# Kernel optimization log

Hardware: AMD Instinct MI355X
Metric: run time of the kernel (lower is better)

Reference implementation:

```python
import jax, jax.numpy as jnp
from jax import lax
import numpy as np

B = 8192   # samples
L = 32     # predicted chars per sample (num_chars[i])
M = 32     # target labels per sample (num_labels[i])
C = 96     # character classes


def _edit_trace(pred, tgt):
    """Levenshtein DP + backtrace for one sample.
    pred: [L] int, tgt: [M] int.
    Returns (ti, tj, valid) of length L+M: 1-based (i,j) positions of the
    diagonal (match/substitute) moves on the optimal edit path, as emitted by
    distance_and_trace; valid masks non-diagonal / out-of-path steps."""
    Ls, Ms = pred.shape[0], tgt.shape[0]
    cost = (pred[:, None] != tgt[None, :]).astype(jnp.int32)  # [L,M]
    row0 = jnp.arange(Ms + 1, dtype=jnp.int32)

    def row_step(prev, crow):
        first = prev[0] + 1
        def col_step(left, z):
            up, diag, c = z
            v = jnp.minimum(jnp.minimum(up + 1, left + 1), diag + c)
            return v, v
        _, rest = lax.scan(col_step, first, (prev[1:], prev[:-1], crow))
        new = jnp.concatenate([first[None], rest])
        return new, new

    _, rows = lax.scan(row_step, row0, cost)
    D = jnp.concatenate([row0[None, :], rows], axis=0)  # [L+1, M+1]

    def bt_step(carry, _):
        i, j = carry
        c = cost[jnp.maximum(i - 1, 0), jnp.maximum(j - 1, 0)]
        dij = D[i, j]
        diag = (i > 0) & (j > 0) & (D[i - 1, j - 1] + c == dij)
        up = (~diag) & (i > 0) & (D[i - 1, j] + 1 == dij)
        left = (~diag) & (~up) & (j > 0)
        ni = i - (diag | up).astype(jnp.int32)
        nj = j - (diag | left).astype(jnp.int32)
        return (ni, nj), (i, j, diag)

    (_, _), (ti, tj, valid) = lax.scan(
        bt_step, (jnp.int32(Ls), jnp.int32(Ms)), None, length=Ls + Ms)
    return ti, tj, valid


def _forward(x, y, num_chars, num_labels):
    b = num_chars.shape[0]
    c = x.shape[1]
    l = x.shape[0] // b
    m = y.shape[0] // b
    logits = x.reshape(b, l, c)          # [B,L,C]
    labels = y.reshape(b, m)             # [B,M]
    pred = jnp.argmax(logits, axis=-1)   # torch.max(x,1) indices
    ti, tj, valid = jax.vmap(_edit_trace)(pred, labels)  # [B, L+M] each
    logp = jax.nn.log_softmax(logits, axis=-1)
    xi = jnp.where(valid, ti - 1, 0)     # trace[:,0]-1 (+ per-sample offset via reshape)
    yi = jnp.where(valid, tj - 1, 0)     # trace[:,1]-1
    lab = jnp.take_along_axis(labels, yi, axis=1)                 # [B,L+M]
    lp = jnp.take_along_axis(logp, xi[..., None], axis=1)         # [B,L+M,C]
    ce = -jnp.take_along_axis(lp, lab[..., None], axis=2)[..., 0]  # [B,L+M]
    cnt = valid.sum(axis=1)
    per_sample = jnp.where(valid, ce, 0.0).sum(axis=1) / jnp.maximum(cnt, 1)
    nonempty = cnt > 0                   # attenuation: skip empty traces
    total = jnp.where(nonempty, per_sample, 0.0).sum()
    return total / nonempty.sum()


def setup_inputs() -> dict:
    key = jax.random.key(0)
    k1, k2 = jax.random.split(key)
    x = jax.random.normal(k1, (B * L, C), dtype=jnp.float32)
    y = jax.random.randint(k2, (B * M,), 0, C, dtype=jnp.int32)
    num_chars = jnp.full((B,), L, dtype=jnp.int32)
    num_labels = jnp.full((B,), M, dtype=jnp.int32)
    return {"x": x, "y": y, "num_chars": num_chars, "num_labels": num_labels}


def reference(x, y, num_chars, num_labels):
    return _forward(x, y, num_chars, num_labels)
```

## Files before the change

### kernel.cpp

```cpp
#include <hip/hip_runtime.h>
#include <stdint.h>

#define BNUM  8192
#define LROWS 32
#define MLAB  32
#define CCLS  96
#define WPB   2
#define SPW   2
#define SPB   (WPB*SPW)
#define NBLK  (BNUM/SPB)

__global__ __launch_bounds__(128, 4) void editloss_main(
    const float* __restrict__ x, const int* __restrict__ y,
    float2* __restrict__ out_ws)
{
    __shared__ float  ceTab[SPB][LROWS * MLAB];
    __shared__ float2 lpS[SPB][LROWS];

    const int w    = threadIdx.x >> 6;
    const int lane = threadIdx.x & 63;
    const int g    = lane >> 5;
    const int u    = lane & 31;
    const int s    = w * SPW + g;
    const int sb   = blockIdx.x * SPB + s;

    const float* xs    = x + (size_t)sb * (LROWS * CCLS);
    const int    lab_u = y[sb * MLAB + u];

    const float4* rowv = (const float4*)(xs + (size_t)u * CCLS);
    float4 buf[24];
#pragma unroll
    for (int k = 0; k < 24; ++k) buf[k] = rowv[k];

    float gbuf[LROWS];
    {
        const float* gcol = xs + lab_u;
#pragma unroll
        for (int r = 0; r < LROWS; ++r) gbuf[r] = gcol[r * CCLS];
    }

    float mA = -1e30f, mB = -1e30f;
    int   iA = 0,      iB = 0;
    float sA = 0.f,    sB = 0.f;
#pragma unroll
    for (int k = 0; k < 12; ++k) {
        const float4 v = buf[k];
        const int base = k * 4;
        if (v.x > mA) { mA = v.x; iA = base + 0; }
        if (v.y > mA) { mA = v.y; iA = base + 1; }
        if (v.z > mA) { mA = v.z; iA = base + 2; }
        if (v.w > mA) { mA = v.w; iA = base + 3; }
        sA += __expf(v.x) + __expf(v.y) + __expf(v.z) + __expf(v.w);
    }
#pragma unroll
    for (int k = 0; k < 12; ++k) {
        const float4 v = buf[12 + k];
        const int base = 48 + k * 4;
        if (v.x > mB) { mB = v.x; iB = base + 0; }
        if (v.y > mB) { mB = v.y; iB = base + 1; }
        if (v.z > mB) { mB = v.z; iB = base + 2; }
        if (v.w > mB) { mB = v.w; iB = base + 3; }
        sB += __expf(v.x) + __expf(v.y) + __expf(v.z) + __expf(v.w);
    }
    const int   idx = (mB > mA) ? iB : iA;
    const float lse = __logf(sA + sB);
    lpS[s][u] = make_float2(lse, (float)idx);

#pragma unroll
    for (int r = 0; r < LROWS; r += 4)
        asm volatile("" : "+v"(gbuf[r]), "+v"(gbuf[r+1]),
                          "+v"(gbuf[r+2]), "+v"(gbuf[r+3]));

    asm volatile("s_waitcnt lgkmcnt(0)" ::: "memory");

#pragma unroll
    for (int r = 0; r < LROWS; ++r) {
        const float2 lp = lpS[s][r];
        const float  ce = lp.x - gbuf[r];
        ceTab[s][r * MLAB + u] = ((int)lp.y == lab_u) ? ce : -ce;
    }
    asm volatile("s_waitcnt lgkmcnt(0)" ::: "memory");

    const int j = u + 1;
    int   prevW = 0;   float prevCE = 0.f;
    int   diagW = 0;   float diagCE = 0.f;
#pragma unroll 4
    for (int d = 1; d <= LROWS + MLAB; ++d) {
        const int   lWs  = __shfl_up(prevW, 1);
        const float lCEs = __shfl_up(prevCE, 1);
        const int i = d - j;
        const int   lW  = (u == 0) ? max(i, 0)     : lWs;
        const float lCE = (u == 0) ? 0.f           : lCEs;
        const int   dW  = (u == 0) ? max(i - 1, 0) : diagW;
        const float dCE = (u == 0) ? 0.f           : diagCE;
        int curW; float curCE;
        if (i <= 0) {
            curW = j; curCE = 0.f;
        } else if (i > LROWS) {
            curW = prevW; curCE = prevCE;
        } else {
            const int uD = prevW & 255, uC = prevW >> 8;
            const int lD = lW & 255,    lC = lW >> 8;
            const int dD = dW & 255,    dC = dW >> 8;
            const float ct  = ceTab[s][(i - 1) * MLAB + u];
            const int   c   = (ct < 0.f) ? 1 : 0;
            const int nD = min(min(uD, lD) + 1, dD + c);
            const bool dg = (dD + c == nD);
            const bool up = !dg && (uD + 1 == nD);
            int nC; float nCE;
            if (dg)      { nC = dC + 1; nCE = dCE + fabsf(ct); }
            else if (up) { nC = uC;     nCE = prevCE;          }
            else         { nC = lC;     nCE = lCE;             }
            curW = nD | (nC << 8);
            curCE = nCE;
        }
        diagW = lWs; diagCE = lCEs;
        prevW = curW; prevCE = curCE;
    }

    if (u == 31) {
        const int cnt = prevW >> 8;
        out_ws[sb] = make_float2((cnt > 0) ? prevCE / (float)cnt : 0.f,
                                 (cnt > 0) ? 1.f : 0.f);
    }
}

__global__ __launch_bounds__(256) void editloss_finalize(
    const float2* __restrict__ ws, float* __restrict__ out)
{
    float s = 0.f, c = 0.f;
    for (int k = threadIdx.x; k < BNUM; k += 256) {
        const float2 v = ws[k];
        s += v.x; c += v.y;
    }
#pragma unroll
    for (int d = 32; d >= 1; d >>= 1) {
        s += __shfl_xor(s, d);
        c += __shfl_xor(c, d);
    }
    __shared__ float ss[4], cc[4];
    const int w = threadIdx.x >> 6, lane = threadIdx.x & 63;
    if (lane == 0) { ss[w] = s; cc[w] = c; }
    __syncthreads();
    if (threadIdx.x == 0) {
        const float S  = ss[0] + ss[1] + ss[2] + ss[3];
        const float C2 = cc[0] + cc[1] + cc[2] + cc[3];
        out[0] = (C2 > 0.f) ? (S / C2) : 0.f;
    }
}

extern "C" void kernel_launch(void* const* d_in, const int* in_sizes, int n_in,
                              void* d_out, int out_size, void* d_ws, size_t ws_size,
                              hipStream_t stream) {
    const float* x = (const float*)d_in[0];
    const int*   y = (const int*)d_in[1];
    float* out = (float*)d_out;

    float2* per_sample = (float2*)d_ws;

    editloss_main<<<NBLK, 128, 0, stream>>>(x, y, per_sample);
    editloss_finalize<<<1, 256, 0, stream>>>(per_sample, out);
}
```

Measured before the change: 171.9 us.

## Split row argmax/logsumexp into a separate wave-parallel kernel

```diff
diff --git a/kernel.cpp b/kernel.cpp
--- a/kernel.cpp
+++ b/kernel.cpp
@@ -5,14 +5,45 @@
 #define LROWS 32
 #define MLAB  32
 #define CCLS  96
+#define SPW   2
 #define WPB   2
-#define SPW   2
 #define SPB   (WPB*SPW)
-#define NBLK  (BNUM/SPB)
+#define NBLKB (BNUM/SPB)
 
-__global__ __launch_bounds__(128, 4) void editloss_main(
+__global__ __launch_bounds__(256) void editloss_rows(
+    const float* __restrict__ x, float2* __restrict__ lpG)
+{
+    const int w    = threadIdx.x >> 6;
+    const int lane = threadIdx.x & 63;
+    const int g    = lane >> 5;
+    const int u    = lane & 31;
+    const int rowbase = blockIdx.x * LROWS + w * 8;
+
+#pragma unroll
+    for (int t = 0; t < 4; ++t) {
+        const int r = rowbase + t * 2 + g;
+        const float* p = x + (size_t)r * CCLS + u * 3;
+        const float v0 = p[0], v1 = p[1], v2 = p[2];
+
+        float m = fmaxf(fmaxf(v0, v1), v2);
+#pragma unroll
+        for (int sft = 16; sft >= 1; sft >>= 1) m = fmaxf(m, __shfl_xor(m, sft));
+        int cand = (v0 == m) ? (u * 3)
+                 : (v1 == m) ? (u * 3 + 1)
+                 : (v2 == m) ? (u * 3 + 2) : 4096;
+#pragma unroll
+        for (int sft = 16; sft >= 1; sft >>= 1) cand = min(cand, __shfl_xor(cand, sft));
+        float se = __expf(v0) + __expf(v1) + __expf(v2);
+#pragma unroll
+        for (int sft = 16; sft >= 1; sft >>= 1) se += __shfl_xor(se, sft);
+
+        if (u == 0) lpG[r] = make_float2(__logf(se), (float)cand);
+    }
+}
+
+__global__ __launch_bounds__(128) void editloss_dp(
     const float* __restrict__ x, const int* __restrict__ y,
-    float2* __restrict__ out_ws)
+    const float2* __restrict__ lpG, float2* __restrict__ out_ws)
 {
     __shared__ float  ceTab[SPB][LROWS * MLAB];
     __shared__ float2 lpS[SPB][LROWS];
@@ -27,10 +58,7 @@
     const float* xs    = x + (size_t)sb * (LROWS * CCLS);
     const int    lab_u = y[sb * MLAB + u];
 
-    const float4* rowv = (const float4*)(xs + (size_t)u * CCLS);
-    float4 buf[24];
-#pragma unroll
-    for (int k = 0; k < 24; ++k) buf[k] = rowv[k];
+    lpS[s][u] = lpG[sb * LROWS + u];
 
     float gbuf[LROWS];
     {
@@ -38,38 +66,6 @@
 #pragma unroll
         for (int r = 0; r < LROWS; ++r) gbuf[r] = gcol[r * CCLS];
     }
-
-    float mA = -1e30f, mB = -1e30f;
-    int   iA = 0,      iB = 0;
-    float sA = 0.f,    sB = 0.f;
-#pragma unroll
-    for (int k = 0; k < 12; ++k) {
-        const float4 v = buf[k];
-        const int base = k * 4;
-        if (v.x > mA) { mA = v.x; iA = base + 0; }
-        if (v.y > mA) { mA = v.y; iA = base + 1; }
-        if (v.z > mA) { mA = v.z; iA = base + 2; }
-        if (v.w > mA) { mA = v.w; iA = base + 3; }
-        sA += __expf(v.x) + __expf(v.y) + __expf(v.z) + __expf(v.w);
-    }
-#pragma unroll
-    for (int k = 0; k < 12; ++k) {
-        const float4 v = buf[12 + k];
-        const int base = 48 + k * 4;
-        if (v.x > mB) { mB = v.x; iB = base + 0; }
-        if (v.y > mB) { mB = v.y; iB = base + 1; }
-        if (v.z > mB) { mB = v.z; iB = base + 2; }
-        if (v.w > mB) { mB = v.w; iB = base + 3; }
-        sB += __expf(v.x) + __expf(v.y) + __expf(v.z) + __expf(v.w);
-    }
-    const int   idx = (mB > mA) ? iB : iA;
-    const float lse = __logf(sA + sB);
-    lpS[s][u] = make_float2(lse, (float)idx);
-
-#pragma unroll
-    for (int r = 0; r < LROWS; r += 4)
-        asm volatile("" : "+v"(gbuf[r]), "+v"(gbuf[r+1]),
-                          "+v"(gbuf[r+2]), "+v"(gbuf[r+3]));
 
     asm volatile("s_waitcnt lgkmcnt(0)" ::: "memory");
 
@@ -156,8 +152,10 @@
     const int*   y = (const int*)d_in[1];
     float* out = (float*)d_out;
 
-    float2* per_sample = (float2*)d_ws;
+    float2* lpG        = (float2*)d_ws;
+    float2* per_sample = lpG + (size_t)BNUM * LROWS;
 
-    editloss_main<<<NBLK, 128, 0, stream>>>(x, y, per_sample);
+    editloss_rows<<<BNUM, 256, 0, stream>>>(x, lpG);
+    editloss_dp<<<NBLKB, 128, 0, stream>>>(x, y, lpG, per_sample);
     editloss_finalize<<<1, 256, 0, stream>>>(per_sample, out);
 }
```

Result: slower. 184.4 us (+7.3%).

## Stage logits through padded LDS tile with coalesced wave-wide loads

Applied to the files above, without the earlier changes.

```diff
diff --git a/kernel.cpp b/kernel.cpp
--- a/kernel.cpp
+++ b/kernel.cpp
@@ -5,81 +5,91 @@
 #define LROWS 32
 #define MLAB  32
 #define CCLS  96
-#define WPB   2
-#define SPW   2
-#define SPB   (WPB*SPW)
+#define CH    16
+#define PAD2  49
+#define WAVES 2
+#define SPWV  2
+#define SPB   (WAVES*SPWV)
 #define NBLK  (BNUM/SPB)
 
-__global__ __launch_bounds__(128, 4) void editloss_main(
+__global__ __launch_bounds__(128) void editloss_main(
     const float* __restrict__ x, const int* __restrict__ y,
     float2* __restrict__ out_ws)
 {
-    __shared__ float  ceTab[SPB][LROWS * MLAB];
-    __shared__ float2 lpS[SPB][LROWS];
+    __shared__ float2 xTile[WAVES][CH * PAD2];
+    __shared__ float  ceTab[WAVES][SPWV][LROWS*MLAB];
+    __shared__ float2 lpS  [WAVES][SPWV][LROWS];
 
-    const int w    = threadIdx.x >> 6;
+    const int wv   = threadIdx.x >> 6;
     const int lane = threadIdx.x & 63;
     const int g    = lane >> 5;
     const int u    = lane & 31;
-    const int s    = w * SPW + g;
-    const int sb   = blockIdx.x * SPB + s;
+    const int sb0  = (blockIdx.x * WAVES + wv) * SPWV;
 
-    const float* xs    = x + (size_t)sb * (LROWS * CCLS);
-    const int    lab_u = y[sb * MLAB + u];
+    for (int si = 0; si < SPWV; ++si) {
+        const float* xs = x + (size_t)(sb0 + si) * (LROWS * CCLS);
+        const int lab_u = y[(sb0 + si) * MLAB + u];
 
-    const float4* rowv = (const float4*)(xs + (size_t)u * CCLS);
-    float4 buf[24];
+        const float4* gsrc = (const float4*)xs;
+        float4 st[12];
 #pragma unroll
-    for (int k = 0; k < 24; ++k) buf[k] = rowv[k];
-
-    float gbuf[LROWS];
-    {
-        const float* gcol = xs + lab_u;
-#pragma unroll
-        for (int r = 0; r < LROWS; ++r) gbuf[r] = gcol[r * CCLS];
-    }
-
-    float mA = -1e30f, mB = -1e30f;
-    int   iA = 0,      iB = 0;
-    float sA = 0.f,    sB = 0.f;
-#pragma unroll
-    for (int k = 0; k < 12; ++k) {
-        const float4 v = buf[k];
-        const int base = k * 4;
-        if (v.x > mA) { mA = v.x; iA = base + 0; }
-        if (v.y > mA) { mA = v.y; iA = base + 1; }
-        if (v.z > mA) { mA = v.z; iA = base + 2; }
-        if (v.w > mA) { mA = v.w; iA = base + 3; }
-        sA += __expf(v.x) + __expf(v.y) + __expf(v.z) + __expf(v.w);
-    }
-#pragma unroll
-    for (int k = 0; k < 12; ++k) {
-        const float4 v = buf[12 + k];
-        const int base = 48 + k * 4;
-        if (v.x > mB) { mB = v.x; iB = base + 0; }
-        if (v.y > mB) { mB = v.y; iB = base + 1; }
-        if (v.z > mB) { mB = v.z; iB = base + 2; }
-        if (v.w > mB) { mB = v.w; iB = base + 3; }
-        sB += __expf(v.x) + __expf(v.y) + __expf(v.z) + __expf(v.w);
-    }
-    const int   idx = (mB > mA) ? iB : iA;
-    const float lse = __logf(sA + sB);
-    lpS[s][u] = make_float2(lse, (float)idx);
+        for (int k = 0; k < 12; ++k) st[k] = gsrc[k * 64 + lane];
 
 #pragma unroll
-    for (int r = 0; r < LROWS; r += 4)
-        asm volatile("" : "+v"(gbuf[r]), "+v"(gbuf[r+1]),
-                          "+v"(gbuf[r+2]), "+v"(gbuf[r+3]));
+        for (int c = 0; c < 2; ++c) {
+            const int r0 = c * CH;
+#pragma unroll
+            for (int k = 0; k < 6; ++k) {
+                const float4 v = st[c * 6 + k];
+                const int f   = k * 64 + lane;
+                const int row = f / 24;
+                const int c4  = f % 24;
+                float2* dst = &xTile[wv][row * PAD2 + c4 * 2];
+                dst[0] = make_float2(v.x, v.y);
+                dst[1] = make_float2(v.z, v.w);
+            }
+            asm volatile("s_waitcnt lgkmcnt(0)" ::: "memory");
 
-    asm volatile("s_waitcnt lgkmcnt(0)" ::: "memory");
+            const int h = lane >> 2;
+            const int o = lane & 3;
+            float2 rv[12];
+#pragma unroll
+            for (int k = 0; k < 12; ++k)
+                rv[k] = xTile[wv][h * PAD2 + o * 12 + k];
+            float m = -1e30f; int idx = 0; float se = 0.f;
+#pragma unroll
+            for (int k = 0; k < 12; ++k) {
+                const int col = o * 24 + k * 2;
+                if (rv[k].x > m) { m = rv[k].x; idx = col;     }
+                if (rv[k].y > m) { m = rv[k].y; idx = col + 1; }
+                se += __expf(rv[k].x) + __expf(rv[k].y);
+            }
+#pragma unroll
+            for (int dd = 1; dd <= 2; dd <<= 1) {
+                const float mo = __shfl_xor(m, dd);
+                const int   io = __shfl_xor(idx, dd);
+                const float so = __shfl_xor(se, dd);
+                if (mo > m || (mo == m && io < idx)) { m = mo; idx = io; }
+                se += so;
+            }
+            if (o == 0)
+                lpS[wv][si][r0 + h] = make_float2(__logf(se), (float)idx);
+            asm volatile("s_waitcnt lgkmcnt(0)" ::: "memory");
 
 #pragma unroll
-    for (int r = 0; r < LROWS; ++r) {
-        const float2 lp = lpS[s][r];
-        const float  ce = lp.x - gbuf[r];
-        ceTab[s][r * MLAB + u] = ((int)lp.y == lab_u) ? ce : -ce;
+            for (int t = 0; t < 8; ++t) {
+                const int rowc = t * 2 + g;
+                const int r    = r0 + rowc;
+                const float2 lp = lpS[wv][si][r];
+                const float  xg =
+                    ((const float*)&xTile[wv][rowc * PAD2])[lab_u];
+                const float  ce = lp.x - xg;
+                ceTab[wv][si][r * MLAB + u] =
+                    ((int)lp.y == lab_u) ? ce : -ce;
+            }
+            asm volatile("s_waitcnt lgkmcnt(0)" ::: "memory");
+        }
     }
-    asm volatile("s_waitcnt lgkmcnt(0)" ::: "memory");
 
     const int j = u + 1;
     int   prevW = 0;   float prevCE = 0.f;
@@ -102,7 +112,7 @@
             const int uD = prevW & 255, uC = prevW >> 8;
             const int lD = lW & 255,    lC = lW >> 8;
             const int dD = dW & 255,    dC = dW >> 8;
-            const float ct  = ceTab[s][(i - 1) * MLAB + u];
+            const float ct  = ceTab[wv][g][(i - 1) * MLAB + u];
             const int   c   = (ct < 0.f) ? 1 : 0;
             const int nD = min(min(uD, lD) + 1, dD + c);
             const bool dg = (dD + c == nD);
@@ -120,8 +130,8 @@
 
     if (u == 31) {
         const int cnt = prevW >> 8;
-        out_ws[sb] = make_float2((cnt > 0) ? prevCE / (float)cnt : 0.f,
-                                 (cnt > 0) ? 1.f : 0.f);
+        out_ws[sb0 + g] = make_float2((cnt > 0) ? prevCE / (float)cnt : 0.f,
+                                      (cnt > 0) ? 1.f : 0.f);
     }
 }
 
```

New measurement: 171.8 us. Within noise of the previous version (-0.0%).

## Map one sample per wavefront and split softmax rows across lane pairs

Applied to the files above, without the earlier changes.

```diff
diff --git a/kernel.cpp b/kernel.cpp
--- a/kernel.cpp
+++ b/kernel.cpp
@@ -5,79 +5,59 @@
 #define LROWS 32
 #define MLAB  32
 #define CCLS  96
-#define WPB   2
-#define SPW   2
-#define SPB   (WPB*SPW)
+#define WPB   4
+#define SPB   WPB
 #define NBLK  (BNUM/SPB)
 
-__global__ __launch_bounds__(128, 4) void editloss_main(
+__global__ __launch_bounds__(256, 8) void editloss_main(
     const float* __restrict__ x, const int* __restrict__ y,
     float2* __restrict__ out_ws)
 {
-    __shared__ float  ceTab[SPB][LROWS * MLAB];
-    __shared__ float2 lpS[SPB][LROWS];
+    __shared__ float  ceTab[WPB][LROWS * MLAB];
+    __shared__ float2 lpS[WPB][LROWS];
 
-    const int w    = threadIdx.x >> 6;
+    const int wv   = threadIdx.x >> 6;
     const int lane = threadIdx.x & 63;
-    const int g    = lane >> 5;
     const int u    = lane & 31;
-    const int s    = w * SPW + g;
-    const int sb   = blockIdx.x * SPB + s;
+    const int sb   = blockIdx.x * WPB + wv;
 
     const float* xs    = x + (size_t)sb * (LROWS * CCLS);
     const int    lab_u = y[sb * MLAB + u];
 
-    const float4* rowv = (const float4*)(xs + (size_t)u * CCLS);
-    float4 buf[24];
+    {
+        const int r = lane >> 1;
+        const int h = lane & 1;
+        const float4* p = (const float4*)(xs + (size_t)r * CCLS + h * 48);
+        float m = -1e30f; int idx = 0; float se = 0.f;
 #pragma unroll
-    for (int k = 0; k < 24; ++k) buf[k] = rowv[k];
-
-    float gbuf[LROWS];
-    {
-        const float* gcol = xs + lab_u;
-#pragma unroll
-        for (int r = 0; r < LROWS; ++r) gbuf[r] = gcol[r * CCLS];
+        for (int k = 0; k < 12; ++k) {
+            const float4 v = p[k];
+            const int base = h * 48 + k * 4;
+            if (v.x > m) { m = v.x; idx = base + 0; }
+            if (v.y > m) { m = v.y; idx = base + 1; }
+            if (v.z > m) { m = v.z; idx = base + 2; }
+            if (v.w > m) { m = v.w; idx = base + 3; }
+            se += __expf(v.x) + __expf(v.y) + __expf(v.z) + __expf(v.w);
+        }
+        const float mo = __shfl_xor(m, 1);
+        const int   io = __shfl_xor(idx, 1);
+        const float so = __shfl_xor(se, 1);
+        if (mo > m || (mo == m && io < idx)) { m = mo; idx = io; }
+        se += so;
+        if (h == 0) lpS[wv][r] = make_float2(__logf(se), (float)idx);
     }
-
-    float mA = -1e30f, mB = -1e30f;
-    int   iA = 0,      iB = 0;
-    float sA = 0.f,    sB = 0.f;
-#pragma unroll
-    for (int k = 0; k < 12; ++k) {
-        const float4 v = buf[k];
-        const int base = k * 4;
-        if (v.x > mA) { mA = v.x; iA = base + 0; }
-        if (v.y > mA) { mA = v.y; iA = base + 1; }
-        if (v.z > mA) { mA = v.z; iA = base + 2; }
-        if (v.w > mA) { mA = v.w; iA = base + 3; }
-        sA += __expf(v.x) + __expf(v.y) + __expf(v.z) + __expf(v.w);
-    }
-#pragma unroll
-    for (int k = 0; k < 12; ++k) {
-        const float4 v = buf[12 + k];
-        const int base = 48 + k * 4;
-        if (v.x > mB) { mB = v.x; iB = base + 0; }
-        if (v.y > mB) { mB = v.y; iB = base + 1; }
-        if (v.z > mB) { mB = v.z; iB = base + 2; }
-        if (v.w > mB) { mB = v.w; iB = base + 3; }
-        sB += __expf(v.x) + __expf(v.y) + __expf(v.z) + __expf(v.w);
-    }
-    const int   idx = (mB > mA) ? iB : iA;
-    const float lse = __logf(sA + sB);
-    lpS[s][u] = make_float2(lse, (float)idx);
-
-#pragma unroll
-    for (int r = 0; r < LROWS; r += 4)
-        asm volatile("" : "+v"(gbuf[r]), "+v"(gbuf[r+1]),
-                          "+v"(gbuf[r+2]), "+v"(gbuf[r+3]));
-
     asm volatile("s_waitcnt lgkmcnt(0)" ::: "memory");
 
+    {
+        const int g2 = lane >> 5;
 #pragma unroll
-    for (int r = 0; r < LROWS; ++r) {
-        const float2 lp = lpS[s][r];
-        const float  ce = lp.x - gbuf[r];
-        ceTab[s][r * MLAB + u] = ((int)lp.y == lab_u) ? ce : -ce;
+        for (int t = 0; t < LROWS / 2; ++t) {
+            const int r = t * 2 + g2;
+            const float2 lp = lpS[wv][r];
+            const float  xg = xs[(size_t)r * CCLS + lab_u];
+            const float  ce = lp.x - xg;
+            ceTab[wv][r * MLAB + u] = ((int)lp.y == lab_u) ? ce : -ce;
+        }
     }
     asm volatile("s_waitcnt lgkmcnt(0)" ::: "memory");
 
@@ -102,7 +82,7 @@
             const int uD = prevW & 255, uC = prevW >> 8;
             const int lD = lW & 255,    lC = lW >> 8;
             const int dD = dW & 255,    dC = dW >> 8;
-            const float ct  = ceTab[s][(i - 1) * MLAB + u];
+            const float ct  = ceTab[wv][(i - 1) * MLAB + u];
             const int   c   = (ct < 0.f) ? 1 : 0;
             const int nD = min(min(uD, lD) + 1, dD + c);
             const bool dg = (dD + c == nD);
@@ -118,7 +98,7 @@
         prevW = curW; prevCE = curCE;
     }
 
-    if (u == 31) {
+    if (lane == 31) {
         const int cnt = prevW >> 8;
         out_ws[sb] = make_float2((cnt > 0) ? prevCE / (float)cnt : 0.f,
                                  (cnt > 0) ? 1.f : 0.f);
@@ -158,6 +138,6 @@
 
     float2* per_sample = (float2*)d_ws;
 
-    editloss_main<<<NBLK, 128, 0, stream>>>(x, y, per_sample);
+    editloss_main<<<NBLK, 256, 0, stream>>>(x, y, per_sample);
     editloss_finalize<<<1, 256, 0, stream>>>(per_sample, out);
 }
```

After: 174.1 us. Within noise of the previous version (+1.3%).
